# Optimization experiments

Hardware: AMD Instinct MI355X
Metric: run time of the kernel (lower is better)

The kernel has to match this reference:

```python
import jax, jax.numpy as jnp
import numpy as np

B, LAT, MEM, IMG = 8192, 256, 200, 128
THRESHOLD = 1.0 / MEM          # sparse-addressing threshold 1/MEM_DIM
EPS_SHRINK = 1e-12             # module epsilon
EPS_COS = 1e-8                 # torch CosineSimilarity default eps
EPS_L1 = 1e-12                 # torch F.normalize default eps


def setup_inputs() -> dict:
    key = jax.random.key(0)
    k1, k2, k3 = jax.random.split(key, 3)
    z = jax.random.normal(k1, (B, LAT), dtype=jnp.float32)          # encoder latent
    memory = jax.random.normal(k2, (MEM, LAT), dtype=jnp.float32) * 0.05  # kaiming-scale memory
    W = jax.random.normal(k3, (IMG * IMG, LAT), dtype=jnp.float32) * 0.02  # linear weight
    b = jnp.zeros((IMG * IMG,), dtype=jnp.float32)
    return {"z": z, "memory": memory, "W": W, "b": b}


def reference(z, memory, W, b):
    # Cosine similarity via normalized matmul (no [B,MEM,LAT] repeat tensors)
    zn = jnp.linalg.norm(z, axis=1, keepdims=True)          # [B,1]
    mn = jnp.linalg.norm(memory, axis=1, keepdims=True)     # [MEM,1]
    logits = (z @ memory.T) / jnp.maximum(zn * mn.T, EPS_COS)  # [B,MEM]
    w = jax.nn.softmax(logits, axis=1)
    # sparse shrinkage: relu(w-t)*w/(|w-t|+eps)
    w = jax.nn.relu(w - THRESHOLD) * w / (jnp.abs(w - THRESHOLD) + EPS_SHRINK)
    # L1 normalize over memory dim
    w = w / jnp.maximum(jnp.sum(jnp.abs(w), axis=1, keepdims=True), EPS_L1)
    z_hat = w @ memory                                      # [B,LAT]
    x_hat = (z_hat @ W.T + b).reshape(-1, 1, IMG, IMG)      # [B,1,128,128]
    return x_hat, z_hat, w
```

## Files before the change

### kernel.cpp

```cpp
#include <hip/hip_runtime.h>
#include <hip/hip_bf16.h>
#include <stdint.h>

#define B_DIM   8192
#define LAT     256
#define MEM_DIM 200
#define MEM_PAD 208
#define MEMT_K  224
#define MEMT_S  232
#define NPIX    16384
#define RPB     8
#define W_QUADS (NPIX * LAT / 4)
#define Z_QUADS (B_DIM * LAT / 4)

typedef short bf16x8 __attribute__((ext_vector_type(8)));
typedef float f32x4  __attribute__((ext_vector_type(4)));

__device__ __forceinline__ float wred_sum(float v) {
#pragma unroll
  for (int m = 32; m; m >>= 1) v += __shfl_xor(v, m, 64);
  return v;
}
__device__ __forceinline__ float wred_max(float v) {
#pragma unroll
  for (int m = 32; m; m >>= 1) v = fmaxf(v, __shfl_xor(v, m, 64));
  return v;
}
__device__ __forceinline__ unsigned short f2bf(float f) {
  unsigned u = __builtin_bit_cast(unsigned, f);
  u = u + 0x7FFFu + ((u >> 16) & 1u);
  return (unsigned short)(u >> 16);
}
__device__ __forceinline__ float bf2f(unsigned short h) {
  return __builtin_bit_cast(float, (unsigned)h << 16);
}
__device__ __forceinline__ void split3(float v, unsigned short& h, unsigned short& m,
                                       unsigned short& l) {
  h = f2bf(v);
  float r1 = v - bf2f(h);
  m = f2bf(r1);
  float r2 = r1 - bf2f(m);
  l = f2bf(r2);
}

__global__ void __launch_bounds__(64) mem_norm_kernel(
    const float* __restrict__ mem, float* __restrict__ mn,
    unsigned short* __restrict__ mem_h, unsigned short* __restrict__ mem_m,
    unsigned short* __restrict__ mem_l,
    unsigned short* __restrict__ memT_h, unsigned short* __restrict__ memT_m,
    unsigned short* __restrict__ memT_l) {
  const int m = blockIdx.x, lane = threadIdx.x;
  if (m >= MEM_DIM) {
    ushort4 zz = {0, 0, 0, 0};
    if (m < MEM_PAD) {
      ((ushort4*)(mem_h + (size_t)m * LAT))[lane] = zz;
      ((ushort4*)(mem_m + (size_t)m * LAT))[lane] = zz;
      ((ushort4*)(mem_l + (size_t)m * LAT))[lane] = zz;
    }
#pragma unroll
    for (int q = 0; q < 4; ++q) {
      const size_t o = (size_t)(lane * 4 + q) * MEMT_S + m;
      memT_h[o] = 0; memT_m[o] = 0; memT_l[o] = 0;
    }
    return;
  }
  float4 v = ((const float4*)(mem + (size_t)m * LAT))[lane];
  ushort4 h, md, l;
  split3(v.x, h.x, md.x, l.x); split3(v.y, h.y, md.y, l.y);
  split3(v.z, h.z, md.z, l.z); split3(v.w, h.w, md.w, l.w);
  ((ushort4*)(mem_h + (size_t)m * LAT))[lane] = h;
  ((ushort4*)(mem_m + (size_t)m * LAT))[lane] = md;
  ((ushort4*)(mem_l + (size_t)m * LAT))[lane] = l;
  const float vv[4] = {v.x, v.y, v.z, v.w};
#pragma unroll
  for (int q = 0; q < 4; ++q) {
    unsigned short th, tm, tl;
    split3(vv[q], th, tm, tl);
    const size_t o = (size_t)(lane * 4 + q) * MEMT_S + m;
    memT_h[o] = th; memT_m[o] = tm; memT_l[o] = tl;
  }
  float ss = v.x * v.x + v.y * v.y + v.z * v.z + v.w * v.w;
  ss = wred_sum(ss);
  if (lane == 0) mn[m] = sqrtf(ss);
}

__global__ void __launch_bounds__(256) prep_kernel(
    const float* __restrict__ W, unsigned short* __restrict__ Wb,
    const float* __restrict__ z, unsigned short* __restrict__ z_h,
    unsigned short* __restrict__ z_m, unsigned short* __restrict__ z_l) {
  const int i = blockIdx.x * 256 + threadIdx.x;
  if (i < W_QUADS) {
    float4 v = ((const float4*)W)[i];
    ushort4 o;
    o.x = f2bf(v.x); o.y = f2bf(v.y); o.z = f2bf(v.z); o.w = f2bf(v.w);
    ((ushort4*)Wb)[i] = o;
  } else {
    const int j = i - W_QUADS;
    float4 v = ((const float4*)z)[j];
    ushort4 h, md, l;
    split3(v.x, h.x, md.x, l.x); split3(v.y, h.y, md.y, l.y);
    split3(v.z, h.z, md.z, l.z); split3(v.w, h.w, md.w, l.w);
    ((ushort4*)z_h)[j] = h;
    ((ushort4*)z_m)[j] = md;
    ((ushort4*)z_l)[j] = l;
  }
}

__global__ void __launch_bounds__(256) row_kernel(
    const float* __restrict__ z, const float* __restrict__ mn_g,
    const unsigned short* __restrict__ z_h, const unsigned short* __restrict__ z_m,
    const unsigned short* __restrict__ z_l,
    const unsigned short* __restrict__ mem_h, const unsigned short* __restrict__ mem_m,
    const unsigned short* __restrict__ mem_l,
    const unsigned short* __restrict__ memT_h, const unsigned short* __restrict__ memT_m,
    const unsigned short* __restrict__ memT_l,
    float* __restrict__ zhat_out, float* __restrict__ w_out,
    unsigned short* __restrict__ zhat_bf) {
  __shared__ float lw[RPB][MEM_DIM];
  __shared__ float mnsh[MEM_DIM];
  __shared__ unsigned short whsh[16 * MEMT_S];
  __shared__ unsigned short wmsh[16 * MEMT_S];
  __shared__ unsigned short wlsh[16 * MEMT_S];

  const int tid = threadIdx.x;
  const int lane = tid & 63;
  const int wid = tid >> 6;
  const int row0 = blockIdx.x * RPB;
  const int fr_ = lane & 15;
  const int kq8 = (lane >> 4) * 8;

  if (tid < MEM_DIM) mnsh[tid] = mn_g[tid];

  float zn[2];
#pragma unroll
  for (int r = 0; r < 2; ++r) {
    const int row = row0 + wid * 2 + r;
    float4 zr = *(const float4*)(z + (size_t)row * LAT + lane * 4);
    float ss = zr.x * zr.x + zr.y * zr.y + zr.z * zr.z + zr.w * zr.w;
    zn[r] = sqrtf(wred_sum(ss));
  }

  {
    const size_t zoff = (size_t)(row0 + (fr_ & 7)) * LAT + kq8;
    const unsigned short* zh_p = z_h + zoff;
    const unsigned short* zm_p = z_m + zoff;
    const unsigned short* zl_p = z_l + zoff;
    for (int nf = wid; nf <= 12; nf += 4) {
      const size_t moff = (size_t)(nf * 16 + fr_) * LAT + kq8;
      const unsigned short* mh_p = mem_h + moff;
      const unsigned short* mm_p = mem_m + moff;
      const unsigned short* ml_p = mem_l + moff;
      f32x4 a = {};
#pragma unroll
      for (int kk = 0; kk < 8; ++kk) {
        bf16x8 zh = *(const bf16x8*)(zh_p + kk * 32);
        bf16x8 zm = *(const bf16x8*)(zm_p + kk * 32);
        bf16x8 zl = *(const bf16x8*)(zl_p + kk * 32);
        bf16x8 mh = *(const bf16x8*)(mh_p + kk * 32);
        bf16x8 mm = *(const bf16x8*)(mm_p + kk * 32);
        bf16x8 ml = *(const bf16x8*)(ml_p + kk * 32);
        a = __builtin_amdgcn_mfma_f32_16x16x32_bf16(zm, mm, a, 0, 0, 0);
        a = __builtin_amdgcn_mfma_f32_16x16x32_bf16(zh, ml, a, 0, 0, 0);
        a = __builtin_amdgcn_mfma_f32_16x16x32_bf16(zl, mh, a, 0, 0, 0);
        a = __builtin_amdgcn_mfma_f32_16x16x32_bf16(zm, mh, a, 0, 0, 0);
        a = __builtin_amdgcn_mfma_f32_16x16x32_bf16(zh, mm, a, 0, 0, 0);
        a = __builtin_amdgcn_mfma_f32_16x16x32_bf16(zh, mh, a, 0, 0, 0);
      }
      const int m = nf * 16 + fr_;
      if (m < MEM_DIM && lane < 32) {
#pragma unroll
        for (int q = 0; q < 4; ++q)
          lw[(lane >> 4) * 4 + q][m] = a[q];
      }
    }
  }
  __syncthreads();

  const float t = 0.005f;
#pragma unroll
  for (int r = 0; r < 2; ++r) {
    const int lr = wid * 2 + r;
    float lg[4];
#pragma unroll
    for (int i = 0; i < 4; ++i) {
      const int m = lane + 64 * i;
      lg[i] = (m < MEM_DIM) ? lw[lr][m] / fmaxf(zn[r] * mnsh[m], 1e-8f) : -1e30f;
    }
    float mx = wred_max(fmaxf(fmaxf(lg[0], lg[1]), fmaxf(lg[2], lg[3])));
    float e[4]; float s = 0.f;
#pragma unroll
    for (int i = 0; i < 4; ++i) {
      const int m = lane + 64 * i;
      e[i] = (m < MEM_DIM) ? expf(lg[i] - mx) : 0.f;
      s += e[i];
    }
    s = wred_sum(s);
    float sv[4]; float l1 = 0.f;
#pragma unroll
    for (int i = 0; i < 4; ++i) {
      const float wv = e[i] / s;
      const float d = wv - t;
      sv[i] = fmaxf(d, 0.f) * wv / (fabsf(d) + 1e-12f);
      l1 += sv[i];
    }
    l1 = wred_sum(l1);
    const float dnm = fmaxf(l1, 1e-12f);
#pragma unroll
    for (int i = 0; i < 4; ++i) {
      const int m = lane + 64 * i;
      if (m < MEM_DIM) {
        const float wn = sv[i] / dnm;
        lw[lr][m] = wn;
        w_out[(size_t)(row0 + lr) * MEM_DIM + m] = wn;
      }
    }
  }
  __syncthreads();

  for (int idx = tid; idx < 16 * MEMT_S; idx += 256) {
    const int lr = idx / MEMT_S, m = idx % MEMT_S;
    const float val = (lr < RPB && m < MEM_DIM) ? lw[lr][m] : 0.f;
    unsigned short h, md, l;
    split3(val, h, md, l);
    whsh[idx] = h; wmsh[idx] = md; wlsh[idx] = l;
  }
  __syncthreads();

  {
    f32x4 zacc[4] = {};
    for (int kk = 0; kk < 7; ++kk) {
      const int ko = kk * 32 + kq8;
      bf16x8 wh = *(const bf16x8*)&whsh[fr_ * MEMT_S + ko];
      bf16x8 wm = *(const bf16x8*)&wmsh[fr_ * MEMT_S + ko];
      bf16x8 wl = *(const bf16x8*)&wlsh[fr_ * MEMT_S + ko];
#pragma unroll
      for (int nf = 0; nf < 4; ++nf) {
        const size_t mo = (size_t)(wid * 64 + nf * 16 + fr_) * MEMT_S + ko;
        bf16x8 th = *(const bf16x8*)(memT_h + mo);
        bf16x8 tm = *(const bf16x8*)(memT_m + mo);
        bf16x8 tl = *(const bf16x8*)(memT_l + mo);
        zacc[nf] = __builtin_amdgcn_mfma_f32_16x16x32_bf16(tm, wm, zacc[nf], 0, 0, 0);
        zacc[nf] = __builtin_amdgcn_mfma_f32_16x16x32_bf16(th, wl, zacc[nf], 0, 0, 0);
        zacc[nf] = __builtin_amdgcn_mfma_f32_16x16x32_bf16(tl, wh, zacc[nf], 0, 0, 0);
        zacc[nf] = __builtin_amdgcn_mfma_f32_16x16x32_bf16(tm, wh, zacc[nf], 0, 0, 0);
        zacc[nf] = __builtin_amdgcn_mfma_f32_16x16x32_bf16(th, wm, zacc[nf], 0, 0, 0);
        zacc[nf] = __builtin_amdgcn_mfma_f32_16x16x32_bf16(th, wh, zacc[nf], 0, 0, 0);
      }
    }
    if (fr_ < RPB) {
      const size_t orow = (size_t)(row0 + fr_) * LAT;
#pragma unroll
      for (int nf = 0; nf < 4; ++nf) {
        const int d0 = wid * 64 + nf * 16 + (lane >> 4) * 4;
        float4 o;
        o.x = zacc[nf][0]; o.y = zacc[nf][1]; o.z = zacc[nf][2]; o.w = zacc[nf][3];
        *(float4*)(zhat_out + orow + d0) = o;
        ushort4 ob;
        ob.x = f2bf(o.x); ob.y = f2bf(o.y); ob.z = f2bf(o.z); ob.w = f2bf(o.w);
        *(ushort4*)(zhat_bf + orow + d0) = ob;
      }
    }
  }
}

#define STAGE(bufbase, t)                                                      \
  {                                                                            \
    const int k0_ = (t) * 32;                                                  \
    _Pragma("unroll")                                                          \
    for (int cc = 0; cc < 2; ++cc) {                                           \
      const int r_ = r0 + cc * 16;                                             \
      __builtin_amdgcn_global_load_lds(                                        \
          (const __attribute__((address_space(1))) void*)(const void*)         \
              (A + (size_t)(brow + r_) * LAT + k0_ + kq),                      \
          (__attribute__((address_space(3))) void*)(void*)                     \
              &smem[(bufbase) + (ch0 + cc) * 1024], 16, 0, 0);                 \
      __builtin_amdgcn_global_load_lds(                                        \
          (const __attribute__((address_space(1))) void*)(const void*)         \
              (Bw + (size_t)(bcol + r_) * LAT + k0_ + kq),                     \
          (__attribute__((address_space(3))) void*)(void*)                     \
              &smem[(bufbase) + 8192 + (ch0 + cc) * 1024], 16, 0, 0);          \
    }                                                                          \
  }

#define GEMM_PROLOG_AND_KLOOP                                                  \
  const int tid = threadIdx.x;                                                 \
  const int lane = tid & 63;                                                   \
  const int wid = tid >> 6;                                                    \
  const int swz = (blockIdx.x & 7) * 1024 + (blockIdx.x >> 3);                 \
  const int st = swz >> 8;                                                     \
  const int loc = swz & 255;                                                   \
  const int tm = (st >> 3) * 16 + (loc & 15);                                  \
  const int tn = (st & 7) * 16 + (loc >> 4);                                   \
  const int brow = tm * 128;                                                   \
  const int bcol = tn * 128;                                                   \
  const int wr = wid >> 1, wc = wid & 1;                                       \
  const int ch0 = wid * 2;                                                     \
  const int r0 = ch0 * 16 + (lane >> 2);                                       \
  const int kq = (lane & 3) * 8;                                               \
  f32x4 acc[4][4] = {};                                                        \
  STAGE(0, 0);                                                                 \
  STAGE(16384, 1);                                                             \
  STAGE(32768, 2);                                                             \
  _Pragma("unroll")                                                            \
  for (int t = 0; t < 8; ++t) {                                                \
    if (t < 6)       asm volatile("s_waitcnt vmcnt(8)" ::: "memory");          \
    else if (t == 6) asm volatile("s_waitcnt vmcnt(4)" ::: "memory");          \
    else             asm volatile("s_waitcnt vmcnt(0)" ::: "memory");          \
    __builtin_amdgcn_sched_barrier(0);                                         \
    __builtin_amdgcn_s_barrier();                                              \
    const int bufb = (t % 3) * 16384;                                          \
    bf16x8 af[4], bfr[4];                                                      \
    _Pragma("unroll")                                                          \
    for (int mf = 0; mf < 4; ++mf)                                             \
      af[mf] = *(const bf16x8*)&smem[bufb + (wr * 64 + mf * 16 + (lane & 15)) * 64 + (lane >> 4) * 16]; \
    _Pragma("unroll")                                                          \
    for (int nf = 0; nf < 4; ++nf)                                             \
      bfr[nf] = *(const bf16x8*)&smem[bufb + 8192 + (wc * 64 + nf * 16 + (lane & 15)) * 64 + (lane >> 4) * 16]; \
    asm volatile("s_waitcnt lgkmcnt(0)" ::: "memory");                         \
    __builtin_amdgcn_sched_barrier(0);                                         \
    __builtin_amdgcn_s_barrier();                                              \
    if (t + 3 < 8) STAGE(((t + 3) % 3) * 16384, t + 3);                        \
    _Pragma("unroll")                                                          \
    for (int mf = 0; mf < 4; ++mf)                                             \
      _Pragma("unroll")                                                        \
      for (int nf = 0; nf < 4; ++nf)                                           \
        acc[mf][nf] = __builtin_amdgcn_mfma_f32_16x16x32_bf16(af[mf], bfr[nf], acc[mf][nf], 0, 0, 0); \
  }

#define TSTRIDE 68
__global__ void __launch_bounds__(256, 3) gemm_xhat_kernel(
    const unsigned short* __restrict__ A, const unsigned short* __restrict__ Bw,
    const float* __restrict__ bias, float* __restrict__ C) {
  __shared__ __align__(16) unsigned char smem[49152];

  GEMM_PROLOG_AND_KLOOP

  __syncthreads();
  float* tt = (float*)(smem + wid * (16 * TSTRIDE * 4));

  const int colq = (lane & 15) * 4;
  const int col0 = bcol + wc * 64 + colq;
  const float4 bv4 = *(const float4*)(bias + col0);

#pragma unroll
  for (int mf = 0; mf < 4; ++mf) {
#pragma unroll
    for (int nf = 0; nf < 4; ++nf) {
      const int cl = nf * 16 + (lane & 15);
#pragma unroll
      for (int q = 0; q < 4; ++q)
        tt[((lane >> 4) * 4 + q) * TSTRIDE + cl] = acc[mf][nf][q];
    }
#pragma unroll
    for (int rr = 0; rr < 4; ++rr) {
      const int rl = rr * 4 + (lane >> 4);
      float4 v = *(const float4*)&tt[rl * TSTRIDE + colq];
      f32x4 ve;
      ve[0] = v.x + bv4.x; ve[1] = v.y + bv4.y;
      ve[2] = v.z + bv4.z; ve[3] = v.w + bv4.w;
      const int row = brow + wr * 64 + mf * 16 + rl;
      __builtin_nontemporal_store(ve, (f32x4*)&C[(size_t)row * NPIX + col0]);
    }
  }
}

extern "C" void kernel_launch(void* const* d_in, const int* in_sizes, int n_in,
                              void* d_out, int out_size, void* d_ws, size_t ws_size,
                              hipStream_t stream) {
  const float* z    = (const float*)d_in[0];
  const float* mem  = (const float*)d_in[1];
  const float* W    = (const float*)d_in[2];
  const float* bias = (const float*)d_in[3];

  float* xhat = (float*)d_out;
  float* zhat = xhat + (size_t)B_DIM * NPIX;
  float* wout = zhat + (size_t)B_DIM * LAT;

  unsigned short* z_h    = (unsigned short*)xhat;
  unsigned short* z_m    = z_h + (size_t)B_DIM * LAT;
  unsigned short* z_l    = z_m + (size_t)B_DIM * LAT;
  unsigned short* mem_h  = z_l + (size_t)B_DIM * LAT;
  unsigned short* mem_m  = mem_h + (size_t)MEM_PAD * LAT;
  unsigned short* mem_l  = mem_m + (size_t)MEM_PAD * LAT;
  unsigned short* memT_h = mem_l + (size_t)MEM_PAD * LAT;
  unsigned short* memT_m = memT_h + (size_t)256 * MEMT_S;
  unsigned short* memT_l = memT_m + (size_t)256 * MEMT_S;

  unsigned short* Wb  = (unsigned short*)d_ws;
  unsigned short* zhb = Wb + (size_t)NPIX * LAT;
  float* mn = (float*)(zhb + (size_t)B_DIM * LAT);

  mem_norm_kernel<<<MEMT_K, 64, 0, stream>>>(mem, mn, mem_h, mem_m, mem_l,
                                             memT_h, memT_m, memT_l);
  prep_kernel<<<(W_QUADS + Z_QUADS) / 256, 256, 0, stream>>>(W, Wb, z, z_h, z_m, z_l);
  row_kernel<<<B_DIM / RPB, 256, 0, stream>>>(z, mn, z_h, z_m, z_l,
                                              mem_h, mem_m, mem_l,
                                              memT_h, memT_m, memT_l,
                                              zhat, wout, zhb);
  gemm_xhat_kernel<<<8192, 256, 0, stream>>>(zhb, Wb, bias, xhat);
}
```

Baseline: 234.3 us.

## Double-buffer the x_hat GEMM and process 16 rows per memory block

```diff
diff --git a/kernel.cpp b/kernel.cpp
--- a/kernel.cpp
+++ b/kernel.cpp
@@ -9,7 +9,7 @@
 #define MEMT_K  224
 #define MEMT_S  232
 #define NPIX    16384
-#define RPB     8
+#define RPB     16
 #define W_QUADS (NPIX * LAT / 4)
 #define Z_QUADS (B_DIM * LAT / 4)
 
@@ -131,17 +131,17 @@
 
   if (tid < MEM_DIM) mnsh[tid] = mn_g[tid];
 
-  float zn[2];
-#pragma unroll
-  for (int r = 0; r < 2; ++r) {
-    const int row = row0 + wid * 2 + r;
+  float zn[4];
+#pragma unroll
+  for (int r = 0; r < 4; ++r) {
+    const int row = row0 + wid * 4 + r;
     float4 zr = *(const float4*)(z + (size_t)row * LAT + lane * 4);
     float ss = zr.x * zr.x + zr.y * zr.y + zr.z * zr.z + zr.w * zr.w;
     zn[r] = sqrtf(wred_sum(ss));
   }
 
   {
-    const size_t zoff = (size_t)(row0 + (fr_ & 7)) * LAT + kq8;
+    const size_t zoff = (size_t)(row0 + fr_) * LAT + kq8;
     const unsigned short* zh_p = z_h + zoff;
     const unsigned short* zm_p = z_m + zoff;
     const unsigned short* zl_p = z_l + zoff;
@@ -167,7 +167,7 @@
         a = __builtin_amdgcn_mfma_f32_16x16x32_bf16(zh, mh, a, 0, 0, 0);
       }
       const int m = nf * 16 + fr_;
-      if (m < MEM_DIM && lane < 32) {
+      if (m < MEM_DIM) {
 #pragma unroll
         for (int q = 0; q < 4; ++q)
           lw[(lane >> 4) * 4 + q][m] = a[q];
@@ -178,8 +178,8 @@
 
   const float t = 0.005f;
 #pragma unroll
-  for (int r = 0; r < 2; ++r) {
-    const int lr = wid * 2 + r;
+  for (int r = 0; r < 4; ++r) {
+    const int lr = wid * 4 + r;
     float lg[4];
 #pragma unroll
     for (int i = 0; i < 4; ++i) {
@@ -219,7 +219,7 @@
 
   for (int idx = tid; idx < 16 * MEMT_S; idx += 256) {
     const int lr = idx / MEMT_S, m = idx % MEMT_S;
-    const float val = (lr < RPB && m < MEM_DIM) ? lw[lr][m] : 0.f;
+    const float val = (m < MEM_DIM) ? lw[lr][m] : 0.f;
     unsigned short h, md, l;
     split3(val, h, md, l);
     whsh[idx] = h; wmsh[idx] = md; wlsh[idx] = l;
@@ -247,21 +247,45 @@
         zacc[nf] = __builtin_amdgcn_mfma_f32_16x16x32_bf16(th, wh, zacc[nf], 0, 0, 0);
       }
     }
-    if (fr_ < RPB) {
-      const size_t orow = (size_t)(row0 + fr_) * LAT;
-#pragma unroll
-      for (int nf = 0; nf < 4; ++nf) {
-        const int d0 = wid * 64 + nf * 16 + (lane >> 4) * 4;
-        float4 o;
-        o.x = zacc[nf][0]; o.y = zacc[nf][1]; o.z = zacc[nf][2]; o.w = zacc[nf][3];
-        *(float4*)(zhat_out + orow + d0) = o;
-        ushort4 ob;
-        ob.x = f2bf(o.x); ob.y = f2bf(o.y); ob.z = f2bf(o.z); ob.w = f2bf(o.w);
-        *(ushort4*)(zhat_bf + orow + d0) = ob;
-      }
-    }
-  }
-}
+    const size_t orow = (size_t)(row0 + fr_) * LAT;
+#pragma unroll
+    for (int nf = 0; nf < 4; ++nf) {
+      const int d0 = wid * 64 + nf * 16 + (lane >> 4) * 4;
+      float4 o;
+      o.x = zacc[nf][0]; o.y = zacc[nf][1]; o.z = zacc[nf][2]; o.w = zacc[nf][3];
+      *(float4*)(zhat_out + orow + d0) = o;
+      ushort4 ob;
+      ob.x = f2bf(o.x); ob.y = f2bf(o.y); ob.z = f2bf(o.z); ob.w = f2bf(o.w);
+      *(ushort4*)(zhat_bf + orow + d0) = ob;
+    }
+  }
+}
+
+#define TSTRIDE 68
+__global__ void __launch_bounds__(256, 4) gemm_xhat_kernel(
+    const unsigned short* __restrict__ A, const unsigned short* __restrict__ Bw,
+    const float* __restrict__ bias, float* __restrict__ C) {
+  __shared__ __align__(16) unsigned char smem[32768];
+
+  const int tid = threadIdx.x;
+  const int lane = tid & 63;
+  const int wid = tid >> 6;
+
+  const int swz = (blockIdx.x & 7) * 1024 + (blockIdx.x >> 3);
+  const int st = swz >> 8;
+  const int loc = swz & 255;
+  const int tm = (st >> 3) * 16 + (loc & 15);
+  const int tn = (st & 7) * 16 + (loc >> 4);
+  const int brow = tm * 128;
+  const int bcol = tn * 128;
+
+  const int wr = wid >> 1, wc = wid & 1;
+
+  const int ch0 = wid * 2;
+  const int r0 = ch0 * 16 + (lane >> 2);
+  const int kq = (lane & 3) * 8;
+
+  f32x4 acc[4][4] = {};
 
 #define STAGE(bufbase, t)                                                      \
   {                                                                            \
@@ -282,58 +306,31 @@
     }                                                                          \
   }
 
-#define GEMM_PROLOG_AND_KLOOP                                                  \
-  const int tid = threadIdx.x;                                                 \
-  const int lane = tid & 63;                                                   \
-  const int wid = tid >> 6;                                                    \
-  const int swz = (blockIdx.x & 7) * 1024 + (blockIdx.x >> 3);                 \
-  const int st = swz >> 8;                                                     \
-  const int loc = swz & 255;                                                   \
-  const int tm = (st >> 3) * 16 + (loc & 15);                                  \
-  const int tn = (st & 7) * 16 + (loc >> 4);                                   \
-  const int brow = tm * 128;                                                   \
-  const int bcol = tn * 128;                                                   \
-  const int wr = wid >> 1, wc = wid & 1;                                       \
-  const int ch0 = wid * 2;                                                     \
-  const int r0 = ch0 * 16 + (lane >> 2);                                       \
-  const int kq = (lane & 3) * 8;                                               \
-  f32x4 acc[4][4] = {};                                                        \
-  STAGE(0, 0);                                                                 \
-  STAGE(16384, 1);                                                             \
-  STAGE(32768, 2);                                                             \
-  _Pragma("unroll")                                                            \
-  for (int t = 0; t < 8; ++t) {                                                \
-    if (t < 6)       asm volatile("s_waitcnt vmcnt(8)" ::: "memory");          \
-    else if (t == 6) asm volatile("s_waitcnt vmcnt(4)" ::: "memory");          \
-    else             asm volatile("s_waitcnt vmcnt(0)" ::: "memory");          \
-    __builtin_amdgcn_sched_barrier(0);                                         \
-    __builtin_amdgcn_s_barrier();                                              \
-    const int bufb = (t % 3) * 16384;                                          \
-    bf16x8 af[4], bfr[4];                                                      \
-    _Pragma("unroll")                                                          \
-    for (int mf = 0; mf < 4; ++mf)                                             \
-      af[mf] = *(const bf16x8*)&smem[bufb + (wr * 64 + mf * 16 + (lane & 15)) * 64 + (lane >> 4) * 16]; \
-    _Pragma("unroll")                                                          \
-    for (int nf = 0; nf < 4; ++nf)                                             \
-      bfr[nf] = *(const bf16x8*)&smem[bufb + 8192 + (wc * 64 + nf * 16 + (lane & 15)) * 64 + (lane >> 4) * 16]; \
-    asm volatile("s_waitcnt lgkmcnt(0)" ::: "memory");                         \
-    __builtin_amdgcn_sched_barrier(0);                                         \
-    __builtin_amdgcn_s_barrier();                                              \
-    if (t + 3 < 8) STAGE(((t + 3) % 3) * 16384, t + 3);                        \
-    _Pragma("unroll")                                                          \
-    for (int mf = 0; mf < 4; ++mf)                                             \
-      _Pragma("unroll")                                                        \
-      for (int nf = 0; nf < 4; ++nf)                                           \
-        acc[mf][nf] = __builtin_amdgcn_mfma_f32_16x16x32_bf16(af[mf], bfr[nf], acc[mf][nf], 0, 0, 0); \
-  }
-
-#define TSTRIDE 68
-__global__ void __launch_bounds__(256, 3) gemm_xhat_kernel(
-    const unsigned short* __restrict__ A, const unsigned short* __restrict__ Bw,
-    const float* __restrict__ bias, float* __restrict__ C) {
-  __shared__ __align__(16) unsigned char smem[49152];
-
-  GEMM_PROLOG_AND_KLOOP
+  STAGE(0, 0);
+  __syncthreads();
+
+#pragma unroll
+  for (int t = 0; t < 8; ++t) {
+    const int bufb = (t & 1) * 16384;
+    if (t < 7) STAGE(bufb ^ 16384, t + 1);
+
+    bf16x8 af[4], bfr[4];
+#pragma unroll
+    for (int mf = 0; mf < 4; ++mf)
+      af[mf] = *(const bf16x8*)&smem[bufb + (wr * 64 + mf * 16 + (lane & 15)) * 64 + (lane >> 4) * 16];
+#pragma unroll
+    for (int nf = 0; nf < 4; ++nf)
+      bfr[nf] = *(const bf16x8*)&smem[bufb + 8192 + (wc * 64 + nf * 16 + (lane & 15)) * 64 + (lane >> 4) * 16];
+
+#pragma unroll
+    for (int mf = 0; mf < 4; ++mf)
+#pragma unroll
+      for (int nf = 0; nf < 4; ++nf)
+        acc[mf][nf] = __builtin_amdgcn_mfma_f32_16x16x32_bf16(af[mf], bfr[nf], acc[mf][nf], 0, 0, 0);
+
+    if (t < 7) __syncthreads();
+  }
+#undef STAGE
 
   __syncthreads();
   float* tt = (float*)(smem + wid * (16 * TSTRIDE * 4));
```

After: 202.5 us (median of 2 runs). 13.6% less time.
